# Optimization experiments

Hardware: AMD Instinct MI355X
Metric: run time of the kernel (lower is better)

The kernel has to match this reference:

```python
import jax, jax.numpy as jnp
import numpy as np

B, N, HID, HEADS = 4, 512, 64, 4
D = HID // HEADS          # head_dim = 16
E_DIM = 1
SCALE = 1.0 / np.sqrt(D)
LN_EPS = 1e-5
NEG = -1e9


def _linear_init(k, fan_in, fan_out):
    lim = 1.0 / np.sqrt(fan_in)
    kw, kb = jax.random.split(k)
    W = jax.random.uniform(kw, (fan_in, fan_out), jnp.float32, -lim, lim)
    b = jax.random.uniform(kb, (fan_out,), jnp.float32, -lim, lim)
    return W, b


def setup_inputs() -> dict:
    key = jax.random.key(0)
    ks = jax.random.split(key, 8)
    W1_w, W1_b = _linear_init(ks[3], HID, HID)
    W2_w, W2_b = _linear_init(ks[4], HID, HID)
    W3_w, W3_b = _linear_init(ks[5], HID, HID)
    W4_w, W4_b = _linear_init(ks[6], HID, HID)
    W5_w, W5_b = _linear_init(ks[7], E_DIM, HID)
    return {
        "x": jax.random.normal(ks[0], (B, N, HID), jnp.float32),
        "adj": jax.random.randint(ks[1], (B, N, N), 0, 2, jnp.int32),
        "edge_features": jax.random.normal(ks[2], (B, N, N, E_DIM), jnp.float32),
        "W1_w": W1_w, "W1_b": W1_b,
        "W2_w": W2_w, "W2_b": W2_b,
        "W3_w": W3_w, "W3_b": W3_b,
        "W4_w": W4_w, "W4_b": W4_b,
        "W5_w": W5_w, "W5_b": W5_b,
        "ln_g": jnp.ones((HID,), jnp.float32),
        "ln_b": jnp.zeros((HID,), jnp.float32),
    }


def _layer_norm(y, g, b):
    m = jnp.mean(y, axis=-1, keepdims=True)
    v = jnp.mean(jnp.square(y - m), axis=-1, keepdims=True)
    return (y - m) * jax.lax.rsqrt(v + LN_EPS) * g + b


def reference(x, adj, edge_features, W1_w, W1_b, W2_w, W2_b, W3_w, W3_b,
              W4_w, W4_b, W5_w, W5_b, ln_g, ln_b):
    b, n, h = x.shape
    self_t = x @ W1_w + W1_b                               # [B,N,HID]
    Q = (x @ W3_w + W3_b).reshape(b, n, HEADS, D)          # [B,N,H,D]
    K = (x @ W4_w + W4_b).reshape(b, n, HEADS, D)          # [B,N,H,D]
    # edge contribution: W5 e_ij -> [B,N,N,H,D] (the big intermediate)
    Ec = (edge_features @ W5_w + W5_b).reshape(b, n, n, HEADS, D)
    # (Q_i . (K_j + E_ij)) split into node-pair GEMM + edge broadcast term
    scores = (jnp.einsum('bihd,bjhd->bhij', Q, K)
              + jnp.einsum('bihd,bijhd->bhij', Q, Ec)) * SCALE  # [B,H,N,N]
    scores = jnp.where(adj[:, None, :, :] == 0, NEG, scores)
    attn = jax.nn.softmax(scores, axis=-1)                 # dropout = identity (eval)
    V = (x @ W2_w + W2_b).reshape(b, n, HEADS, D)          # [B,N,H,D]
    msg = jnp.einsum('bhij,bjhd->bihd', attn, V).reshape(b, n, h)
    return _layer_norm(x + self_t + msg, ln_g, ln_b)
```

## Files before the change

### kernel.cpp

```cpp
#include <hip/hip_runtime.h>

#define B 4
#define N 512
#define HID 64
#define HEADS 4
#define DH 16
#define SCALE 0.25f
#define NEG (-1e9f)
#define LN_EPS 1e-5f

constexpr int ROWS = B * N;
constexpr size_t OFF_ST  = 0;
constexpr size_t OFF_Q   = (size_t)ROWS * HID;
constexpr size_t OFF_K   = 2 * OFF_Q;
constexpr size_t OFF_V   = 3 * OFF_Q;
constexpr size_t OFF_MSG = 4 * OFF_Q;

__global__ __launch_bounds__(256) void proj_kernel(
    const float* __restrict__ x,
    const float* __restrict__ W1w, const float* __restrict__ W1b,
    const float* __restrict__ W2w, const float* __restrict__ W2b,
    const float* __restrict__ W3w, const float* __restrict__ W3b,
    const float* __restrict__ W4w, const float* __restrict__ W4b,
    float* __restrict__ ws)
{
  __shared__ float xsT[64 * 8];
  const int t = threadIdx.x;
  const int rows0 = blockIdx.x * 8;

  if (t < 128) {
    const float4 v = *(const float4*)&x[(size_t)rows0 * HID + t * 4];
    const int r = t >> 4;
    const int k0 = (t & 15) * 4;
    xsT[(k0 + 0) * 8 + r] = v.x;
    xsT[(k0 + 1) * 8 + r] = v.y;
    xsT[(k0 + 2) * 8 + r] = v.z;
    xsT[(k0 + 3) * 8 + r] = v.w;
  }
  __syncthreads();

  const int m = t >> 6;
  const int c = t & 63;
  const float* Ww; const float* Wb; size_t off;
  if      (m == 0) { Ww = W1w; Wb = W1b; off = OFF_ST; }
  else if (m == 1) { Ww = W3w; Wb = W3b; off = OFF_Q;  }
  else if (m == 2) { Ww = W4w; Wb = W4b; off = OFF_K;  }
  else             { Ww = W2w; Wb = W2b; off = OFF_V;  }

  float acc[8];
#pragma unroll
  for (int r = 0; r < 8; ++r) acc[r] = 0.f;

#pragma unroll 16
  for (int k = 0; k < 64; ++k) {
    const float w = Ww[(k << 6) + c];
    const float* xr = &xsT[k * 8];
    const float4 a0 = *(const float4*)(xr);
    const float4 a1 = *(const float4*)(xr + 4);
    acc[0] = fmaf(a0.x, w, acc[0]); acc[1] = fmaf(a0.y, w, acc[1]);
    acc[2] = fmaf(a0.z, w, acc[2]); acc[3] = fmaf(a0.w, w, acc[3]);
    acc[4] = fmaf(a1.x, w, acc[4]); acc[5] = fmaf(a1.y, w, acc[5]);
    acc[6] = fmaf(a1.z, w, acc[6]); acc[7] = fmaf(a1.w, w, acc[7]);
  }

  const float bias = Wb[c];
  const size_t base = off + (size_t)rows0 * HID + c;
#pragma unroll
  for (int r = 0; r < 8; ++r)
    ws[base + (size_t)r * HID] = acc[r] + bias;
}

__global__ __launch_bounds__(256, 2) void attn_kernel(
    const int*   __restrict__ adj,
    const float* __restrict__ efeat,
    const float* __restrict__ W5w, const float* __restrict__ W5b,
    float* __restrict__ ws)
{
  __shared__ float Ksh[N * 20];
  __shared__ float Vsh[N * 20];

  const int it = blockIdx.x, h = blockIdx.y, b = blockIdx.z;
  const int t = threadIdx.x;
  const int g  = t & 15;
  const int il = t >> 4;
  const int iA = it * 32 + il;
  const int iB = iA + 16;

  const float* Qb = ws + OFF_Q;
  const float* Kb = ws + OFF_K;
  const float* Vb = ws + OFF_V;
  float* msg = ws + OFF_MSG;

  {
    const int jj = t >> 2;
    const int dq = (t & 3) << 2;
#pragma unroll
    for (int p = 0; p < 8; ++p) {
      const int j = jj + (p << 6);
      const size_t gb = ((size_t)(b * N + j)) * HID + h * DH + dq;
      *(float4*)&Ksh[j * 20 + dq] = *(const float4*)&Kb[gb];
      *(float4*)&Vsh[j * 20 + dq] = *(const float4*)&Vb[gb];
    }
  }

  const float4 w50 = *(const float4*)&W5w[h * DH];
  const float4 w51 = *(const float4*)&W5w[h * DH + 4];
  const float4 w52 = *(const float4*)&W5w[h * DH + 8];
  const float4 w53 = *(const float4*)&W5w[h * DH + 12];
  const float4 b50 = *(const float4*)&W5b[h * DH];
  const float4 b51 = *(const float4*)&W5b[h * DH + 4];
  const float4 b52 = *(const float4*)&W5b[h * DH + 8];
  const float4 b53 = *(const float4*)&W5b[h * DH + 12];

  float4 qA0, qA1, qA2, qA3, qB0, qB1, qB2, qB3;
  float qw5A, qb5A, qw5B, qb5B;
  {
    const float* qr = Qb + ((size_t)(b * N + iA)) * HID + h * DH;
    qA0 = *(const float4*)(qr);     qA1 = *(const float4*)(qr + 4);
    qA2 = *(const float4*)(qr + 8); qA3 = *(const float4*)(qr + 12);
    qw5A = qA0.x*w50.x + qA0.y*w50.y + qA0.z*w50.z + qA0.w*w50.w
         + qA1.x*w51.x + qA1.y*w51.y + qA1.z*w51.z + qA1.w*w51.w
         + qA2.x*w52.x + qA2.y*w52.y + qA2.z*w52.z + qA2.w*w52.w
         + qA3.x*w53.x + qA3.y*w53.y + qA3.z*w53.z + qA3.w*w53.w;
    qb5A = qA0.x*b50.x + qA0.y*b50.y + qA0.z*b50.z + qA0.w*b50.w
         + qA1.x*b51.x + qA1.y*b51.y + qA1.z*b51.z + qA1.w*b51.w
         + qA2.x*b52.x + qA2.y*b52.y + qA2.z*b52.z + qA2.w*b52.w
         + qA3.x*b53.x + qA3.y*b53.y + qA3.z*b53.z + qA3.w*b53.w;
  }
  {
    const float* qr = Qb + ((size_t)(b * N + iB)) * HID + h * DH;
    qB0 = *(const float4*)(qr);     qB1 = *(const float4*)(qr + 4);
    qB2 = *(const float4*)(qr + 8); qB3 = *(const float4*)(qr + 12);
    qw5B = qB0.x*w50.x + qB0.y*w50.y + qB0.z*w50.z + qB0.w*w50.w
         + qB1.x*w51.x + qB1.y*w51.y + qB1.z*w51.z + qB1.w*w51.w
         + qB2.x*w52.x + qB2.y*w52.y + qB2.z*w52.z + qB2.w*w52.w
         + qB3.x*w53.x + qB3.y*w53.y + qB3.z*w53.z + qB3.w*w53.w;
    qb5B = qB0.x*b50.x + qB0.y*b50.y + qB0.z*b50.z + qB0.w*b50.w
         + qB1.x*b51.x + qB1.y*b51.y + qB1.z*b51.z + qB1.w*b51.w
         + qB2.x*b52.x + qB2.y*b52.y + qB2.z*b52.z + qB2.w*b52.w
         + qB3.x*b53.x + qB3.y*b53.y + qB3.z*b53.z + qB3.w*b53.w;
  }

  __syncthreads();

  const int*   adjA = adj   + ((size_t)(b * N + iA)) * N;
  const int*   adjB = adj   + ((size_t)(b * N + iB)) * N;
  const float* eA   = efeat + ((size_t)(b * N + iA)) * N;
  const float* eB   = efeat + ((size_t)(b * N + iB)) * N;

  float sA[32], sB[32];
#pragma unroll
  for (int jj = 0; jj < 32; ++jj) {
    const int j = g + (jj << 4);
    const int   aA = adjA[j], aB = adjB[j];
    const float evA = eA[j],  evB = eB[j];
    const float* kr = &Ksh[j * 20];
    const float4 k0 = *(const float4*)(kr);
    const float4 k1 = *(const float4*)(kr + 4);
    const float4 k2 = *(const float4*)(kr + 8);
    const float4 k3 = *(const float4*)(kr + 12);

    float a0 = qA0.x*k0.x + qA0.y*k0.y + qA0.z*k0.z + qA0.w*k0.w;
    a0 = fmaf(qA1.x,k1.x, fmaf(qA1.y,k1.y, fmaf(qA1.z,k1.z, fmaf(qA1.w,k1.w, a0))));
    a0 = fmaf(qA2.x,k2.x, fmaf(qA2.y,k2.y, fmaf(qA2.z,k2.z, fmaf(qA2.w,k2.w, a0))));
    a0 = fmaf(qA3.x,k3.x, fmaf(qA3.y,k3.y, fmaf(qA3.z,k3.z, fmaf(qA3.w,k3.w, a0))));
    float b0 = qB0.x*k0.x + qB0.y*k0.y + qB0.z*k0.z + qB0.w*k0.w;
    b0 = fmaf(qB1.x,k1.x, fmaf(qB1.y,k1.y, fmaf(qB1.z,k1.z, fmaf(qB1.w,k1.w, b0))));
    b0 = fmaf(qB2.x,k2.x, fmaf(qB2.y,k2.y, fmaf(qB2.z,k2.z, fmaf(qB2.w,k2.w, b0))));
    b0 = fmaf(qB3.x,k3.x, fmaf(qB3.y,k3.y, fmaf(qB3.z,k3.z, fmaf(qB3.w,k3.w, b0))));

    const float scA = (a0 + evA * qw5A + qb5A) * SCALE;
    const float scB = (b0 + evB * qw5B + qb5B) * SCALE;
    sA[jj] = (aA == 0) ? NEG : scA;
    sB[jj] = (aB == 0) ? NEG : scB;
  }

  float mA0 = sA[0], mA1 = sA[1], mA2 = sA[2], mA3 = sA[3];
  float mB0 = sB[0], mB1 = sB[1], mB2 = sB[2], mB3 = sB[3];
#pragma unroll
  for (int jj = 4; jj < 32; jj += 4) {
    mA0 = fmaxf(mA0, sA[jj]);     mA1 = fmaxf(mA1, sA[jj + 1]);
    mA2 = fmaxf(mA2, sA[jj + 2]); mA3 = fmaxf(mA3, sA[jj + 3]);
    mB0 = fmaxf(mB0, sB[jj]);     mB1 = fmaxf(mB1, sB[jj + 1]);
    mB2 = fmaxf(mB2, sB[jj + 2]); mB3 = fmaxf(mB3, sB[jj + 3]);
  }
  float MA = fmaxf(fmaxf(mA0, mA1), fmaxf(mA2, mA3));
  float MB = fmaxf(fmaxf(mB0, mB1), fmaxf(mB2, mB3));
#pragma unroll
  for (int o = 1; o < 16; o <<= 1) {
    MA = fmaxf(MA, __shfl_xor(MA, o, 16));
    MB = fmaxf(MB, __shfl_xor(MB, o, 16));
  }

  float lA = 0.f, lB = 0.f;
  float accA[16], accB[16];
#pragma unroll
  for (int d = 0; d < 16; ++d) { accA[d] = 0.f; accB[d] = 0.f; }

#pragma unroll
  for (int jj = 0; jj < 32; ++jj) {
    const int j = g + (jj << 4);
    const float pA = __expf(sA[jj] - MA);
    const float pB = __expf(sB[jj] - MB);
    lA += pA; lB += pB;
    const float* vr = &Vsh[j * 20];
    const float4 v0 = *(const float4*)(vr);
    const float4 v1 = *(const float4*)(vr + 4);
    const float4 v2 = *(const float4*)(vr + 8);
    const float4 v3 = *(const float4*)(vr + 12);
    accA[0] = fmaf(pA,v0.x,accA[0]); accA[1] = fmaf(pA,v0.y,accA[1]);
    accA[2] = fmaf(pA,v0.z,accA[2]); accA[3] = fmaf(pA,v0.w,accA[3]);
    accA[4] = fmaf(pA,v1.x,accA[4]); accA[5] = fmaf(pA,v1.y,accA[5]);
    accA[6] = fmaf(pA,v1.z,accA[6]); accA[7] = fmaf(pA,v1.w,accA[7]);
    accA[8] = fmaf(pA,v2.x,accA[8]); accA[9] = fmaf(pA,v2.y,accA[9]);
    accA[10]= fmaf(pA,v2.z,accA[10]);accA[11]= fmaf(pA,v2.w,accA[11]);
    accA[12]= fmaf(pA,v3.x,accA[12]);accA[13]= fmaf(pA,v3.y,accA[13]);
    accA[14]= fmaf(pA,v3.z,accA[14]);accA[15]= fmaf(pA,v3.w,accA[15]);
    accB[0] = fmaf(pB,v0.x,accB[0]); accB[1] = fmaf(pB,v0.y,accB[1]);
    accB[2] = fmaf(pB,v0.z,accB[2]); accB[3] = fmaf(pB,v0.w,accB[3]);
    accB[4] = fmaf(pB,v1.x,accB[4]); accB[5] = fmaf(pB,v1.y,accB[5]);
    accB[6] = fmaf(pB,v1.z,accB[6]); accB[7] = fmaf(pB,v1.w,accB[7]);
    accB[8] = fmaf(pB,v2.x,accB[8]); accB[9] = fmaf(pB,v2.y,accB[9]);
    accB[10]= fmaf(pB,v2.z,accB[10]);accB[11]= fmaf(pB,v2.w,accB[11]);
    accB[12]= fmaf(pB,v3.x,accB[12]);accB[13]= fmaf(pB,v3.y,accB[13]);
    accB[14]= fmaf(pB,v3.z,accB[14]);accB[15]= fmaf(pB,v3.w,accB[15]);
  }

#pragma unroll
  for (int o = 1; o < 16; o <<= 1) {
    lA += __shfl_xor(lA, o, 16);
    lB += __shfl_xor(lB, o, 16);
  }

  __syncthreads();
  float* P = Ksh;
  const int baseA = (il * 16 + g) * 20;
  const int baseB = ((il + 16) * 16 + g) * 20;
  *(float4*)&P[baseA+ 0] = make_float4(accA[0],  accA[1],  accA[2],  accA[3]);
  *(float4*)&P[baseA+ 4] = make_float4(accA[4],  accA[5],  accA[6],  accA[7]);
  *(float4*)&P[baseA+ 8] = make_float4(accA[8],  accA[9],  accA[10], accA[11]);
  *(float4*)&P[baseA+12] = make_float4(accA[12], accA[13], accA[14], accA[15]);
  *(float4*)&P[baseB+ 0] = make_float4(accB[0],  accB[1],  accB[2],  accB[3]);
  *(float4*)&P[baseB+ 4] = make_float4(accB[4],  accB[5],  accB[6],  accB[7]);
  *(float4*)&P[baseB+ 8] = make_float4(accB[8],  accB[9],  accB[10], accB[11]);
  *(float4*)&P[baseB+12] = make_float4(accB[12], accB[13], accB[14], accB[15]);
  __syncthreads();

  float sumA = 0.f, sumB = 0.f;
#pragma unroll
  for (int gp = 0; gp < 16; ++gp) {
    sumA += P[(il * 16 + gp) * 20 + g];
    sumB += P[((il + 16) * 16 + gp) * 20 + g];
  }
  msg[((size_t)(b * N + iA)) * HID + h * DH + g] = sumA * (1.0f / lA);
  msg[((size_t)(b * N + iB)) * HID + h * DH + g] = sumB * (1.0f / lB);
}

__global__ __launch_bounds__(256) void ln_kernel(
    const float* __restrict__ x, const float* __restrict__ ws,
    const float* __restrict__ gamma, const float* __restrict__ beta,
    float* __restrict__ out)
{
  const int t = threadIdx.x;
  const int lane = t & 63;
  const int row = blockIdx.x * 4 + (t >> 6);
  const size_t idx = (size_t)row * HID + lane;
  const float* ST  = ws + OFF_ST;
  const float* MSG = ws + OFF_MSG;

  const float v = x[idx] + ST[idx] + MSG[idx];
  float mu = v;
#pragma unroll
  for (int o = 1; o < 64; o <<= 1) mu += __shfl_xor(mu, o, 64);
  mu *= (1.0f / 64.0f);
  const float dv = v - mu;
  float var = dv * dv;
#pragma unroll
  for (int o = 1; o < 64; o <<= 1) var += __shfl_xor(var, o, 64);
  var *= (1.0f / 64.0f);
  out[idx] = dv * rsqrtf(var + LN_EPS) * gamma[lane] + beta[lane];
}

extern "C" void kernel_launch(void* const* d_in, const int* in_sizes, int n_in,
                              void* d_out, int out_size, void* d_ws, size_t ws_size,
                              hipStream_t stream)
{
  const float* x   = (const float*)d_in[0];
  const int*   adj = (const int*)d_in[1];
  const float* ef  = (const float*)d_in[2];
  const float* W1w = (const float*)d_in[3];
  const float* W1b = (const float*)d_in[4];
  const float* W2w = (const float*)d_in[5];
  const float* W2b = (const float*)d_in[6];
  const float* W3w = (const float*)d_in[7];
  const float* W3b = (const float*)d_in[8];
  const float* W4w = (const float*)d_in[9];
  const float* W4b = (const float*)d_in[10];
  const float* W5w = (const float*)d_in[11];
  const float* W5b = (const float*)d_in[12];
  const float* lng = (const float*)d_in[13];
  const float* lnb = (const float*)d_in[14];
  float* ws  = (float*)d_ws;
  float* out = (float*)d_out;

  proj_kernel<<<ROWS / 8, 256, 0, stream>>>(x, W1w, W1b, W2w, W2b, W3w, W3b, W4w, W4b, ws);
  attn_kernel<<<dim3(16, HEADS, B), 256, 0, stream>>>(adj, ef, W5w, W5b, ws);
  ln_kernel<<<ROWS / 4, 256, 0, stream>>>(x, ws, lng, lnb, out);
}
```

Before: 25.36 us.

## Split attention over key chunks with flash-decoding style partial softmax merge

```diff
diff --git a/kernel.cpp b/kernel.cpp
--- a/kernel.cpp
+++ b/kernel.cpp
@@ -6,7 +6,6 @@
 #define HEADS 4
 #define DH 16
 #define SCALE 0.25f
-#define NEG (-1e9f)
 #define LN_EPS 1e-5f
 
 constexpr int ROWS = B * N;
@@ -14,7 +13,7 @@
 constexpr size_t OFF_Q   = (size_t)ROWS * HID;
 constexpr size_t OFF_K   = 2 * OFF_Q;
 constexpr size_t OFF_V   = 3 * OFF_Q;
-constexpr size_t OFF_MSG = 4 * OFF_Q;
+constexpr size_t OFF_PART= 4 * OFF_Q;
 
 __global__ __launch_bounds__(256) void proj_kernel(
     const float* __restrict__ x,
@@ -24,18 +23,18 @@
     const float* __restrict__ W4w, const float* __restrict__ W4b,
     float* __restrict__ ws)
 {
-  __shared__ float xsT[64 * 8];
+  __shared__ float xsT[64 * 4];
   const int t = threadIdx.x;
-  const int rows0 = blockIdx.x * 8;
-
-  if (t < 128) {
+  const int rows0 = blockIdx.x * 4;
+
+  if (t < 64) {
     const float4 v = *(const float4*)&x[(size_t)rows0 * HID + t * 4];
     const int r = t >> 4;
     const int k0 = (t & 15) * 4;
-    xsT[(k0 + 0) * 8 + r] = v.x;
-    xsT[(k0 + 1) * 8 + r] = v.y;
-    xsT[(k0 + 2) * 8 + r] = v.z;
-    xsT[(k0 + 3) * 8 + r] = v.w;
+    xsT[(k0 + 0) * 4 + r] = v.x;
+    xsT[(k0 + 1) * 4 + r] = v.y;
+    xsT[(k0 + 2) * 4 + r] = v.z;
+    xsT[(k0 + 3) * 4 + r] = v.w;
   }
   __syncthreads();
 
@@ -47,39 +46,37 @@
   else if (m == 2) { Ww = W4w; Wb = W4b; off = OFF_K;  }
   else             { Ww = W2w; Wb = W2b; off = OFF_V;  }
 
-  float acc[8];
-#pragma unroll
-  for (int r = 0; r < 8; ++r) acc[r] = 0.f;
+  float acc[4];
+#pragma unroll
+  for (int r = 0; r < 4; ++r) acc[r] = 0.f;
 
 #pragma unroll 16
   for (int k = 0; k < 64; ++k) {
     const float w = Ww[(k << 6) + c];
-    const float* xr = &xsT[k * 8];
-    const float4 a0 = *(const float4*)(xr);
-    const float4 a1 = *(const float4*)(xr + 4);
+    const float4 a0 = *(const float4*)&xsT[k * 4];
     acc[0] = fmaf(a0.x, w, acc[0]); acc[1] = fmaf(a0.y, w, acc[1]);
     acc[2] = fmaf(a0.z, w, acc[2]); acc[3] = fmaf(a0.w, w, acc[3]);
-    acc[4] = fmaf(a1.x, w, acc[4]); acc[5] = fmaf(a1.y, w, acc[5]);
-    acc[6] = fmaf(a1.z, w, acc[6]); acc[7] = fmaf(a1.w, w, acc[7]);
   }
 
   const float bias = Wb[c];
   const size_t base = off + (size_t)rows0 * HID + c;
 #pragma unroll
-  for (int r = 0; r < 8; ++r)
+  for (int r = 0; r < 4; ++r)
     ws[base + (size_t)r * HID] = acc[r] + bias;
 }
 
-__global__ __launch_bounds__(256, 2) void attn_kernel(
+__global__ __launch_bounds__(256, 4) void attn_kernel(
     const int*   __restrict__ adj,
     const float* __restrict__ efeat,
     const float* __restrict__ W5w, const float* __restrict__ W5b,
     float* __restrict__ ws)
 {
-  __shared__ float Ksh[N * 20];
-  __shared__ float Vsh[N * 20];
-
-  const int it = blockIdx.x, h = blockIdx.y, b = blockIdx.z;
+  __shared__ float KV[512 * 20];
+
+  const int it = blockIdx.x, h = blockIdx.y;
+  const int b  = blockIdx.z >> 2;
+  const int qt = blockIdx.z & 3;
+  const int j0 = qt << 7;
   const int t = threadIdx.x;
   const int g  = t & 15;
   const int il = t >> 4;
@@ -89,17 +86,21 @@
   const float* Qb = ws + OFF_Q;
   const float* Kb = ws + OFF_K;
   const float* Vb = ws + OFF_V;
-  float* msg = ws + OFF_MSG;
-
-  {
-    const int jj = t >> 2;
+  float* part = ws + OFF_PART;
+
+  float* Ksh = KV;
+  float* Vsh = KV + 2560;
+
+  {
+    const int sj = t >> 2;
     const int dq = (t & 3) << 2;
 #pragma unroll
-    for (int p = 0; p < 8; ++p) {
-      const int j = jj + (p << 6);
-      const size_t gb = ((size_t)(b * N + j)) * HID + h * DH + dq;
-      *(float4*)&Ksh[j * 20 + dq] = *(const float4*)&Kb[gb];
-      *(float4*)&Vsh[j * 20 + dq] = *(const float4*)&Vb[gb];
+    for (int p = 0; p < 2; ++p) {
+      const int j  = sj + (p << 6);
+      const int sr = ((j & 3) << 5) | (j >> 2);
+      const size_t gb = ((size_t)(b * N + j0 + j)) * HID + h * DH + dq;
+      *(float4*)&Ksh[sr * 20 + dq] = *(const float4*)&Kb[gb];
+      *(float4*)&Vsh[sr * 20 + dq] = *(const float4*)&Vb[gb];
     }
   }
 
@@ -141,51 +142,72 @@
          + qB3.x*b53.x + qB3.y*b53.y + qB3.z*b53.z + qB3.w*b53.w;
   }
 
+  float cA[8], cB[8];
+  {
+    const int*   aR = adj   + ((size_t)(b * N + iA)) * N + j0;
+    const float* eR = efeat + ((size_t)(b * N + iA)) * N + j0;
+    const int4   a0 = *(const int4*)&aR[4 * g];
+    const int4   a1 = *(const int4*)&aR[4 * g + 64];
+    const float4 e0 = *(const float4*)&eR[4 * g];
+    const float4 e1 = *(const float4*)&eR[4 * g + 64];
+    cA[0] = a0.x ? fmaf(e0.x, qw5A, qb5A) : -4e9f;
+    cA[1] = a0.y ? fmaf(e0.y, qw5A, qb5A) : -4e9f;
+    cA[2] = a0.z ? fmaf(e0.z, qw5A, qb5A) : -4e9f;
+    cA[3] = a0.w ? fmaf(e0.w, qw5A, qb5A) : -4e9f;
+    cA[4] = a1.x ? fmaf(e1.x, qw5A, qb5A) : -4e9f;
+    cA[5] = a1.y ? fmaf(e1.y, qw5A, qb5A) : -4e9f;
+    cA[6] = a1.z ? fmaf(e1.z, qw5A, qb5A) : -4e9f;
+    cA[7] = a1.w ? fmaf(e1.w, qw5A, qb5A) : -4e9f;
+  }
+  {
+    const int*   aR = adj   + ((size_t)(b * N + iB)) * N + j0;
+    const float* eR = efeat + ((size_t)(b * N + iB)) * N + j0;
+    const int4   a0 = *(const int4*)&aR[4 * g];
+    const int4   a1 = *(const int4*)&aR[4 * g + 64];
+    const float4 e0 = *(const float4*)&eR[4 * g];
+    const float4 e1 = *(const float4*)&eR[4 * g + 64];
+    cB[0] = a0.x ? fmaf(e0.x, qw5B, qb5B) : -4e9f;
+    cB[1] = a0.y ? fmaf(e0.y, qw5B, qb5B) : -4e9f;
+    cB[2] = a0.z ? fmaf(e0.z, qw5B, qb5B) : -4e9f;
+    cB[3] = a0.w ? fmaf(e0.w, qw5B, qb5B) : -4e9f;
+    cB[4] = a1.x ? fmaf(e1.x, qw5B, qb5B) : -4e9f;
+    cB[5] = a1.y ? fmaf(e1.y, qw5B, qb5B) : -4e9f;
+    cB[6] = a1.z ? fmaf(e1.z, qw5B, qb5B) : -4e9f;
+    cB[7] = a1.w ? fmaf(e1.w, qw5B, qb5B) : -4e9f;
+  }
+
   __syncthreads();
 
-  const int*   adjA = adj   + ((size_t)(b * N + iA)) * N;
-  const int*   adjB = adj   + ((size_t)(b * N + iB)) * N;
-  const float* eA   = efeat + ((size_t)(b * N + iA)) * N;
-  const float* eB   = efeat + ((size_t)(b * N + iB)) * N;
-
-  float sA[32], sB[32];
-#pragma unroll
-  for (int jj = 0; jj < 32; ++jj) {
-    const int j = g + (jj << 4);
-    const int   aA = adjA[j], aB = adjB[j];
-    const float evA = eA[j],  evB = eB[j];
-    const float* kr = &Ksh[j * 20];
-    const float4 k0 = *(const float4*)(kr);
-    const float4 k1 = *(const float4*)(kr + 4);
-    const float4 k2 = *(const float4*)(kr + 8);
-    const float4 k3 = *(const float4*)(kr + 12);
-
-    float a0 = qA0.x*k0.x + qA0.y*k0.y + qA0.z*k0.z + qA0.w*k0.w;
-    a0 = fmaf(qA1.x,k1.x, fmaf(qA1.y,k1.y, fmaf(qA1.z,k1.z, fmaf(qA1.w,k1.w, a0))));
-    a0 = fmaf(qA2.x,k2.x, fmaf(qA2.y,k2.y, fmaf(qA2.z,k2.z, fmaf(qA2.w,k2.w, a0))));
-    a0 = fmaf(qA3.x,k3.x, fmaf(qA3.y,k3.y, fmaf(qA3.z,k3.z, fmaf(qA3.w,k3.w, a0))));
-    float b0 = qB0.x*k0.x + qB0.y*k0.y + qB0.z*k0.z + qB0.w*k0.w;
-    b0 = fmaf(qB1.x,k1.x, fmaf(qB1.y,k1.y, fmaf(qB1.z,k1.z, fmaf(qB1.w,k1.w, b0))));
-    b0 = fmaf(qB2.x,k2.x, fmaf(qB2.y,k2.y, fmaf(qB2.z,k2.z, fmaf(qB2.w,k2.w, b0))));
-    b0 = fmaf(qB3.x,k3.x, fmaf(qB3.y,k3.y, fmaf(qB3.z,k3.z, fmaf(qB3.w,k3.w, b0))));
-
-    const float scA = (a0 + evA * qw5A + qb5A) * SCALE;
-    const float scB = (b0 + evB * qw5B + qb5B) * SCALE;
-    sA[jj] = (aA == 0) ? NEG : scA;
-    sB[jj] = (aB == 0) ? NEG : scB;
-  }
-
-  float mA0 = sA[0], mA1 = sA[1], mA2 = sA[2], mA3 = sA[3];
-  float mB0 = sB[0], mB1 = sB[1], mB2 = sB[2], mB3 = sB[3];
-#pragma unroll
-  for (int jj = 4; jj < 32; jj += 4) {
-    mA0 = fmaxf(mA0, sA[jj]);     mA1 = fmaxf(mA1, sA[jj + 1]);
-    mA2 = fmaxf(mA2, sA[jj + 2]); mA3 = fmaxf(mA3, sA[jj + 3]);
-    mB0 = fmaxf(mB0, sB[jj]);     mB1 = fmaxf(mB1, sB[jj + 1]);
-    mB2 = fmaxf(mB2, sB[jj + 2]); mB3 = fmaxf(mB3, sB[jj + 3]);
-  }
-  float MA = fmaxf(fmaxf(mA0, mA1), fmaxf(mA2, mA3));
-  float MB = fmaxf(fmaxf(mB0, mB1), fmaxf(mB2, mB3));
+  float sA[8], sB[8];
+#pragma unroll
+  for (int q = 0; q < 2; ++q) {
+#pragma unroll
+    for (int r = 0; r < 4; ++r) {
+      const int idx = (q << 2) | r;
+      const int sr = (r << 5) | (g + (q << 4));
+      const float* kr = &Ksh[sr * 20];
+      const float4 k0 = *(const float4*)(kr);
+      const float4 k1 = *(const float4*)(kr + 4);
+      const float4 k2 = *(const float4*)(kr + 8);
+      const float4 k3 = *(const float4*)(kr + 12);
+      float a0 = qA0.x*k0.x + qA0.y*k0.y + qA0.z*k0.z + qA0.w*k0.w;
+      a0 = fmaf(qA1.x,k1.x, fmaf(qA1.y,k1.y, fmaf(qA1.z,k1.z, fmaf(qA1.w,k1.w, a0))));
+      a0 = fmaf(qA2.x,k2.x, fmaf(qA2.y,k2.y, fmaf(qA2.z,k2.z, fmaf(qA2.w,k2.w, a0))));
+      a0 = fmaf(qA3.x,k3.x, fmaf(qA3.y,k3.y, fmaf(qA3.z,k3.z, fmaf(qA3.w,k3.w, a0))));
+      float b0 = qB0.x*k0.x + qB0.y*k0.y + qB0.z*k0.z + qB0.w*k0.w;
+      b0 = fmaf(qB1.x,k1.x, fmaf(qB1.y,k1.y, fmaf(qB1.z,k1.z, fmaf(qB1.w,k1.w, b0))));
+      b0 = fmaf(qB2.x,k2.x, fmaf(qB2.y,k2.y, fmaf(qB2.z,k2.z, fmaf(qB2.w,k2.w, b0))));
+      b0 = fmaf(qB3.x,k3.x, fmaf(qB3.y,k3.y, fmaf(qB3.z,k3.z, fmaf(qB3.w,k3.w, b0))));
+      sA[idx] = (a0 + cA[idx]) * SCALE;
+      sB[idx] = (b0 + cB[idx]) * SCALE;
+    }
+  }
+
+  float a4A[4], a4B[4];
+#pragma unroll
+  for (int k = 0; k < 4; ++k) { a4A[k] = fmaxf(sA[k], sA[k+4]); a4B[k] = fmaxf(sB[k], sB[k+4]); }
+  float MA = fmaxf(fmaxf(a4A[0], a4A[1]), fmaxf(a4A[2], a4A[3]));
+  float MB = fmaxf(fmaxf(a4B[0], a4B[1]), fmaxf(a4B[2], a4B[3]));
 #pragma unroll
   for (int o = 1; o < 16; o <<= 1) {
     MA = fmaxf(MA, __shfl_xor(MA, o, 16));
@@ -198,32 +220,36 @@
   for (int d = 0; d < 16; ++d) { accA[d] = 0.f; accB[d] = 0.f; }
 
 #pragma unroll
-  for (int jj = 0; jj < 32; ++jj) {
-    const int j = g + (jj << 4);
-    const float pA = __expf(sA[jj] - MA);
-    const float pB = __expf(sB[jj] - MB);
-    lA += pA; lB += pB;
-    const float* vr = &Vsh[j * 20];
-    const float4 v0 = *(const float4*)(vr);
-    const float4 v1 = *(const float4*)(vr + 4);
-    const float4 v2 = *(const float4*)(vr + 8);
-    const float4 v3 = *(const float4*)(vr + 12);
-    accA[0] = fmaf(pA,v0.x,accA[0]); accA[1] = fmaf(pA,v0.y,accA[1]);
-    accA[2] = fmaf(pA,v0.z,accA[2]); accA[3] = fmaf(pA,v0.w,accA[3]);
-    accA[4] = fmaf(pA,v1.x,accA[4]); accA[5] = fmaf(pA,v1.y,accA[5]);
-    accA[6] = fmaf(pA,v1.z,accA[6]); accA[7] = fmaf(pA,v1.w,accA[7]);
-    accA[8] = fmaf(pA,v2.x,accA[8]); accA[9] = fmaf(pA,v2.y,accA[9]);
-    accA[10]= fmaf(pA,v2.z,accA[10]);accA[11]= fmaf(pA,v2.w,accA[11]);
-    accA[12]= fmaf(pA,v3.x,accA[12]);accA[13]= fmaf(pA,v3.y,accA[13]);
-    accA[14]= fmaf(pA,v3.z,accA[14]);accA[15]= fmaf(pA,v3.w,accA[15]);
-    accB[0] = fmaf(pB,v0.x,accB[0]); accB[1] = fmaf(pB,v0.y,accB[1]);
-    accB[2] = fmaf(pB,v0.z,accB[2]); accB[3] = fmaf(pB,v0.w,accB[3]);
-    accB[4] = fmaf(pB,v1.x,accB[4]); accB[5] = fmaf(pB,v1.y,accB[5]);
-    accB[6] = fmaf(pB,v1.z,accB[6]); accB[7] = fmaf(pB,v1.w,accB[7]);
-    accB[8] = fmaf(pB,v2.x,accB[8]); accB[9] = fmaf(pB,v2.y,accB[9]);
-    accB[10]= fmaf(pB,v2.z,accB[10]);accB[11]= fmaf(pB,v2.w,accB[11]);
-    accB[12]= fmaf(pB,v3.x,accB[12]);accB[13]= fmaf(pB,v3.y,accB[13]);
-    accB[14]= fmaf(pB,v3.z,accB[14]);accB[15]= fmaf(pB,v3.w,accB[15]);
+  for (int q = 0; q < 2; ++q) {
+#pragma unroll
+    for (int r = 0; r < 4; ++r) {
+      const int idx = (q << 2) | r;
+      const float pA = __expf(sA[idx] - MA);
+      const float pB = __expf(sB[idx] - MB);
+      lA += pA; lB += pB;
+      const int sr = (r << 5) | (g + (q << 4));
+      const float* vr = &Vsh[sr * 20];
+      const float4 v0 = *(const float4*)(vr);
+      const float4 v1 = *(const float4*)(vr + 4);
+      const float4 v2 = *(const float4*)(vr + 8);
+      const float4 v3 = *(const float4*)(vr + 12);
+      accA[0] = fmaf(pA,v0.x,accA[0]); accA[1] = fmaf(pA,v0.y,accA[1]);
+      accA[2] = fmaf(pA,v0.z,accA[2]); accA[3] = fmaf(pA,v0.w,accA[3]);
+      accA[4] = fmaf(pA,v1.x,accA[4]); accA[5] = fmaf(pA,v1.y,accA[5]);
+      accA[6] = fmaf(pA,v1.z,accA[6]); accA[7] = fmaf(pA,v1.w,accA[7]);
+      accA[8] = fmaf(pA,v2.x,accA[8]); accA[9] = fmaf(pA,v2.y,accA[9]);
+      accA[10]= fmaf(pA,v2.z,accA[10]);accA[11]= fmaf(pA,v2.w,accA[11]);
+      accA[12]= fmaf(pA,v3.x,accA[12]);accA[13]= fmaf(pA,v3.y,accA[13]);
+      accA[14]= fmaf(pA,v3.z,accA[14]);accA[15]= fmaf(pA,v3.w,accA[15]);
+      accB[0] = fmaf(pB,v0.x,accB[0]); accB[1] = fmaf(pB,v0.y,accB[1]);
+      accB[2] = fmaf(pB,v0.z,accB[2]); accB[3] = fmaf(pB,v0.w,accB[3]);
+      accB[4] = fmaf(pB,v1.x,accB[4]); accB[5] = fmaf(pB,v1.y,accB[5]);
+      accB[6] = fmaf(pB,v1.z,accB[6]); accB[7] = fmaf(pB,v1.w,accB[7]);
+      accB[8] = fmaf(pB,v2.x,accB[8]); accB[9] = fmaf(pB,v2.y,accB[9]);
+      accB[10]= fmaf(pB,v2.z,accB[10]);accB[11]= fmaf(pB,v2.w,accB[11]);
+      accB[12]= fmaf(pB,v3.x,accB[12]);accB[13]= fmaf(pB,v3.y,accB[13]);
+      accB[14]= fmaf(pB,v3.z,accB[14]);accB[15]= fmaf(pB,v3.w,accB[15]);
+    }
   }
 
 #pragma unroll
@@ -233,7 +259,7 @@
   }
 
   __syncthreads();
-  float* P = Ksh;
+  float* P = KV;
   const int baseA = (il * 16 + g) * 20;
   const int baseB = ((il + 16) * 16 + g) * 20;
   *(float4*)&P[baseA+ 0] = make_float4(accA[0],  accA[1],  accA[2],  accA[3]);
@@ -252,8 +278,12 @@
     sumA += P[(il * 16 + gp) * 20 + g];
     sumB += P[((il + 16) * 16 + gp) * 20 + g];
   }
-  msg[((size_t)(b * N + iA)) * HID + h * DH + g] = sumA * (1.0f / lA);
-  msg[((size_t)(b * N + iB)) * HID + h * DH + g] = sumB * (1.0f / lB);
+
+  float* recA = part + ((((size_t)(b * N + iA)) * HEADS + h) * 4 + qt) * 18;
+  float* recB = part + ((((size_t)(b * N + iB)) * HEADS + h) * 4 + qt) * 18;
+  recA[g] = sumA;
+  recB[g] = sumB;
+  if (g == 0) { recA[16] = MA; recA[17] = lA; recB[16] = MB; recB[17] = lB; }
 }
 
 __global__ __launch_bounds__(256) void ln_kernel(
@@ -265,10 +295,24 @@
   const int lane = t & 63;
   const int row = blockIdx.x * 4 + (t >> 6);
   const size_t idx = (size_t)row * HID + lane;
-  const float* ST  = ws + OFF_ST;
-  const float* MSG = ws + OFF_MSG;
-
-  const float v = x[idx] + ST[idx] + MSG[idx];
+  const float* ST   = ws + OFF_ST;
+  const float* part = ws + OFF_PART;
+
+  const int h = lane >> 4;
+  const int d = lane & 15;
+  const float* rec = part + (((size_t)row * HEADS + h) * 4) * 18;
+  const float m0 = rec[16],      l0 = rec[17];
+  const float m1 = rec[18 + 16], l1 = rec[18 + 17];
+  const float m2 = rec[36 + 16], l2 = rec[36 + 17];
+  const float m3 = rec[54 + 16], l3 = rec[54 + 17];
+  const float M  = fmaxf(fmaxf(m0, m1), fmaxf(m2, m3));
+  const float w0 = __expf(m0 - M), w1 = __expf(m1 - M);
+  const float w2 = __expf(m2 - M), w3 = __expf(m3 - M);
+  const float num = rec[d]*w0 + rec[18+d]*w1 + rec[36+d]*w2 + rec[54+d]*w3;
+  const float den = l0*w0 + l1*w1 + l2*w2 + l3*w3;
+  const float msg = num / den;
+
+  const float v = x[idx] + ST[idx] + msg;
   float mu = v;
 #pragma unroll
   for (int o = 1; o < 64; o <<= 1) mu += __shfl_xor(mu, o, 64);
@@ -303,7 +347,7 @@
   float* ws  = (float*)d_ws;
   float* out = (float*)d_out;
 
-  proj_kernel<<<ROWS / 8, 256, 0, stream>>>(x, W1w, W1b, W2w, W2b, W3w, W3b, W4w, W4b, ws);
-  attn_kernel<<<dim3(16, HEADS, B), 256, 0, stream>>>(adj, ef, W5w, W5b, ws);
+  proj_kernel<<<ROWS / 4, 256, 0, stream>>>(x, W1w, W1b, W2w, W2b, W3w, W3b, W4w, W4b, ws);
+  attn_kernel<<<dim3(16, HEADS, B * 4), 256, 0, stream>>>(adj, ef, W5w, W5b, ws);
   ln_kernel<<<ROWS / 4, 256, 0, stream>>>(x, ws, lng, lnb, out);
 }
```

Measured after the change: 22.67 us. -10.6%, faster.
